# Kernel optimization log

Measured on AMD Instinct MI355X. Metric: run time of the kernel, lower is better.

Reference implementation:

```python
import jax, jax.numpy as jnp
import numpy as np

N_USER = 50000
N_ITEM = 100000
EMB = 64
NNZ = 1200000
BATCH = 4096
RATE = 0.1          # node_dropout[0]
N_LAYERS = 4        # len(layer_size); make_hop needs >=4 hops for 5 prefix means
N_NODES = N_USER + N_ITEM


def setup_inputs() -> dict:
    key = jax.random.key(0)
    ks = jax.random.split(key, 12)
    return {
        "user_emb": jax.random.normal(ks[0], (N_USER, EMB), dtype=jnp.float32) * 0.1,
        "item_emb": jax.random.normal(ks[1], (N_ITEM, EMB), dtype=jnp.float32) * 0.1,
        "adj_vals": jax.random.uniform(ks[2], (NNZ,), dtype=jnp.float32),
        "drop_u": jax.random.uniform(ks[3], (NNZ,), dtype=jnp.float32),
        "adj_rows": jax.random.randint(ks[4], (NNZ,), 0, N_NODES, dtype=jnp.int32),
        "adj_cols": jax.random.randint(ks[5], (NNZ,), 0, N_NODES, dtype=jnp.int32),
        "users": jax.random.randint(ks[6], (BATCH,), 0, N_USER, dtype=jnp.int32),
        "pos_items": jax.random.randint(ks[7], (BATCH,), 0, N_ITEM, dtype=jnp.int32),
        "neg_items": jax.random.randint(ks[8], (BATCH,), 0, N_ITEM, dtype=jnp.int32),
        "u_a": jax.random.randint(ks[9], (BATCH,), 0, 5, dtype=jnp.int32),
        "p_a": jax.random.randint(ks[10], (BATCH,), 0, 5, dtype=jnp.int32),
        "n_a": jax.random.randint(ks[11], (BATCH,), 0, 5, dtype=jnp.int32),
        "index": 0,
    }


def _make_hop(user_emb, item_emb, adj_vals, drop_u, adj_rows, adj_cols):
    # sparse dropout: floor(1 - rate + u) gives a 0/1 keep mask; rescale by 1/(1-rate).
    mask = jnp.floor((1.0 - RATE) + drop_u)
    vals = adj_vals * mask * (1.0 / (1.0 - RATE))
    ego = jnp.concatenate([user_emb, item_emb], axis=0)  # [N, d]
    all_embs = [ego]
    for _ in range(N_LAYERS):
        # SpMM: out[r] = sum_e vals[e] * ego[cols[e]] for rows[e] == r
        msgs = vals[:, None] * ego[adj_cols]             # [nnz, d]
        ego = jax.ops.segment_sum(msgs, adj_rows, num_segments=N_NODES)
        all_embs.append(ego)
    # prefix means over hops 0..i
    result = [all_embs[0]]
    running = all_embs[0]
    for i in range(1, 5):
        running = running + all_embs[i]
        result.append(running / float(i + 1))
    return jnp.stack(result)  # [5, N, d]


def reference(user_emb, item_emb, adj_vals, drop_u, adj_rows, adj_cols,
              users, pos_items, neg_items, u_a, p_a, n_a, index):
    embed = _make_hop(user_emb, item_emb, adj_vals, drop_u, adj_rows, adj_cols)
    n_user = user_emb.shape[0]
    if index == 0:
        u = embed[u_a, users]
        p = embed[p_a, pos_items + n_user]
        n = embed[n_a, neg_items + n_user]
    else:
        u = embed[u_a, users + n_user]
        p = embed[p_a, pos_items]
        n = embed[n_a, neg_items]
    return (u, p, n)
```

## Files before the change

kernel.cpp:

```cpp
#include <hip/hip_runtime.h>
#include <stdint.h>

#define N_USER_C  50000
#define N_ITEM_C  100000
#define N_NODES_C 150000
#define EMB_C     64
#define NNZ_C     1200000
#define BATCH_C   4096

#define BKT_SHIFT 9
#define BKT_ROWS  (1 << BKT_SHIFT)
#define NB        ((N_NODES_C + BKT_ROWS - 1) / BKT_ROWS)
#define CH        8192
#define NBLK      ((NNZ_C + CH - 1) / CH)
#define N2        (NB * NBLK)
#define COL_MASK  0x3FFFF

typedef _Float16 h16;
typedef _Float16 h16x4 __attribute__((ext_vector_type(4)));
typedef _Float16 h16x8 __attribute__((ext_vector_type(8)));

__global__ __launch_bounds__(1024) void k_bin_count(const float* __restrict__ du,
                                                    const int* __restrict__ rows,
                                                    int* __restrict__ cnt2) {
    __shared__ int bk[NB];
    int t = threadIdx.x, blk = blockIdx.x;
    for (int i = t; i < NB; i += 1024) bk[i] = 0;
    __syncthreads();
    int base = blk * CH;
    for (int i = 0; i < CH; i += 1024) {
        int e = base + i + t;
        if (e < NNZ_C && floorf(0.9f + du[e]) != 0.0f)
            atomicAdd(&bk[rows[e] >> BKT_SHIFT], 1);
    }
    __syncthreads();
    for (int i = t; i < NB; i += 1024) cnt2[i * NBLK + blk] = bk[i];
}

__global__ __launch_bounds__(256) void k_btot(const int* __restrict__ cnt2,
                                              int* __restrict__ btot) {
    __shared__ int red[256];
    int t = threadIdx.x, i = blockIdx.x;
    red[t] = (t < NBLK) ? cnt2[i * NBLK + t] : 0;
    __syncthreads();
    for (int off = 128; off > 0; off >>= 1) {
        if (t < off) red[t] += red[t + off];
        __syncthreads();
    }
    if (t == 0) btot[i] = red[0];
}

__global__ __launch_bounds__(512) void k_bbase(const int* __restrict__ btot,
                                               int* __restrict__ bbase,
                                               int* __restrict__ base2,
                                               int* __restrict__ row_start) {
    __shared__ int sh[512];
    int t = threadIdx.x;
    int v0 = (t < NB) ? btot[t] : 0;
    sh[t] = v0;
    __syncthreads();
    for (int off = 1; off < 512; off <<= 1) {
        int v = (t >= off) ? sh[t - off] : 0;
        __syncthreads();
        sh[t] += v;
        __syncthreads();
    }
    if (t < NB) bbase[t] = sh[t] - v0;
    if (t == 511) {
        base2[N2] = sh[511];
        row_start[N_NODES_C] = sh[511];
    }
}

__global__ __launch_bounds__(256) void k_bscan(const int* __restrict__ cnt2,
                                               const int* __restrict__ bbase,
                                               int* __restrict__ base2) {
    __shared__ int sh[256];
    int t = threadIdx.x, i = blockIdx.x;
    int v0 = (t < NBLK) ? cnt2[i * NBLK + t] : 0;
    sh[t] = v0;
    __syncthreads();
    for (int off = 1; off < 256; off <<= 1) {
        int v = (t >= off) ? sh[t - off] : 0;
        __syncthreads();
        sh[t] += v;
        __syncthreads();
    }
    if (t < NBLK) base2[i * NBLK + t] = bbase[i] + sh[t] - v0;
}

__global__ __launch_bounds__(1024) void k_bin_write(const float* __restrict__ av,
                                                    const float* __restrict__ du,
                                                    const int* __restrict__ rows,
                                                    const int* __restrict__ cols,
                                                    const int* __restrict__ base2,
                                                    int2* __restrict__ ev) {
    __shared__ int cur[NB];
    int t = threadIdx.x, blk = blockIdx.x;
    for (int i = t; i < NB; i += 1024) cur[i] = base2[i * NBLK + blk];
    __syncthreads();
    int base = blk * CH;
    for (int i = 0; i < CH; i += 1024) {
        int e = base + i + t;
        if (e < NNZ_C) {
            float m = floorf(0.9f + du[e]);
            if (m != 0.0f) {
                float v = av[e] * m * (float)(1.0 / 0.9);
                int r = rows[e];
                int pos = atomicAdd(&cur[r >> BKT_SHIFT], 1);
                int2 p;
                p.x = ((r & (BKT_ROWS - 1)) << 18) | cols[e];
                p.y = __float_as_int(v);
                ev[pos] = p;
            }
        }
    }
}

__global__ __launch_bounds__(256) void k_bucket_sort(const int2* __restrict__ ev,
                                                     const int* __restrict__ base2,
                                                     int2* __restrict__ ep,
                                                     int* __restrict__ row_start) {
    __shared__ int rowcnt[BKT_ROWS];
    __shared__ int cursor[BKT_ROWS];
    __shared__ int tsum[256];
    int t = threadIdx.x, k = blockIdx.x;
    int rowBase = k << BKT_SHIFT;
    int bstart = base2[k * NBLK];
    int bend   = base2[(k + 1) * NBLK];
    for (int i = t; i < BKT_ROWS; i += 256) rowcnt[i] = 0;
    __syncthreads();
    for (int e = bstart + t; e < bend; e += 256)
        atomicAdd(&rowcnt[((unsigned)ev[e].x) >> 18], 1);
    __syncthreads();
    int a = rowcnt[2 * t], b = rowcnt[2 * t + 1];
    tsum[t] = a + b;
    __syncthreads();
    for (int off = 1; off < 256; off <<= 1) {
        int v = (t >= off) ? tsum[t - off] : 0;
        __syncthreads();
        tsum[t] += v;
        __syncthreads();
    }
    int excl = tsum[t] - (a + b);
    cursor[2 * t]     = excl;
    cursor[2 * t + 1] = excl + a;
    int gr = rowBase + 2 * t;
    if (gr < N_NODES_C)     row_start[gr]     = bstart + excl;
    if (gr + 1 < N_NODES_C) row_start[gr + 1] = bstart + excl + a;
    __syncthreads();
    for (int e = bstart + t; e < bend; e += 256) {
        int2 p = ev[e];
        int rl = ((unsigned)p.x) >> 18;
        int slot = atomicAdd(&cursor[rl], 1);
        p.x &= COL_MASK;
        ep[bstart + slot] = p;
    }
}

__global__ __launch_bounds__(256) void k_tohalf(const float4* __restrict__ ue,
                                                const float4* __restrict__ ie,
                                                h16x4* __restrict__ dst) {
    const int totalU = N_USER_C * EMB_C / 4;
    const int total  = N_NODES_C * EMB_C / 4;
    int stride = gridDim.x * blockDim.x;
    for (int i = blockIdx.x * blockDim.x + threadIdx.x; i < total; i += stride) {
        float4 v = (i < totalU) ? ue[i] : ie[i - totalU];
        h16x4 h;
        h[0] = (h16)v.x; h[1] = (h16)v.y; h[2] = (h16)v.z; h[3] = (h16)v.w;
        dst[i] = h;
    }
}

__global__ __launch_bounds__(256) void k_spmm8d(const int* __restrict__ rs,
                                                const int2* __restrict__ ep,
                                                const h16x8* __restrict__ ego,
                                                h16x8* __restrict__ nxt,
                                                const int* __restrict__ flag) {
    int wid  = (blockIdx.x * blockDim.x + threadIdx.x) >> 6;
    int lane = threadIdx.x & 63;
    if (wid >= N_NODES_C) return;
    if (flag && flag[wid] == 0) return;
    int start = rs[wid];
    int end   = rs[wid + 1];
    int slot = lane >> 3;
    int q    = lane & 7;
    float acc[8] = {0.f, 0.f, 0.f, 0.f, 0.f, 0.f, 0.f, 0.f};
    #pragma unroll 2
    for (int it = start + slot; it < end; it += 8) {
        long long raw = __builtin_nontemporal_load((const long long*)(ep + it));
        int   c = (int)(raw & 0xFFFFFFFFLL);
        float v = __int_as_float((int)(raw >> 32));
        h16x8 g = ego[((int64_t)(c << 3)) + q];
        #pragma unroll
        for (int i = 0; i < 8; ++i) acc[i] += v * (float)g[i];
    }
    #pragma unroll
    for (int m = 8; m <= 32; m <<= 1) {
        #pragma unroll
        for (int i = 0; i < 8; ++i) acc[i] += __shfl_xor(acc[i], m);
    }
    if (lane < 8) {
        h16x8 h;
        #pragma unroll
        for (int i = 0; i < 8; ++i) h[i] = (h16)acc[i];
        nxt[(int64_t)wid * 8 + q] = h;
    }
}

__global__ __launch_bounds__(256) void k_flags(const int* __restrict__ rs,
                                               const int2* __restrict__ ep,
                                               int* __restrict__ flag,
                                               const int* __restrict__ users,
                                               const int* __restrict__ pos,
                                               const int* __restrict__ neg,
                                               const int* __restrict__ ua,
                                               const int* __restrict__ pa,
                                               const int* __restrict__ na,
                                               const int* __restrict__ indexp) {
    int wid  = (blockIdx.x * blockDim.x + threadIdx.x) >> 6;
    int lane = threadIdx.x & 63;
    if (wid >= 3 * BATCH_C) return;
    int s = wid >> 12;
    int j = wid & (BATCH_C - 1);
    int a = (s == 0) ? ua[j] : (s == 1) ? pa[j] : na[j];
    if (a < 3) return;
    int idx0 = indexp[0];
    int row;
    if (s == 0)      row = users[j] + (idx0 ? N_USER_C : 0);
    else if (s == 1) row = pos[j]   + (idx0 ? 0 : N_USER_C);
    else             row = neg[j]   + (idx0 ? 0 : N_USER_C);
    if (lane == 0) flag[row] = 1;
    if (a == 4) {
        int start = rs[row], end = rs[row + 1];
        for (int e = start + lane; e < end; e += 64)
            flag[ep[e].x] = 1;
    }
}

__global__ __launch_bounds__(256) void k_spmm_g4(const int* __restrict__ rs,
                                                 const int2* __restrict__ ep,
                                                 const h16x4* __restrict__ ego,
                                                 float* __restrict__ out,
                                                 const int* __restrict__ users,
                                                 const int* __restrict__ pos,
                                                 const int* __restrict__ neg,
                                                 const int* __restrict__ ua,
                                                 const int* __restrict__ pa,
                                                 const int* __restrict__ na,
                                                 const int* __restrict__ indexp) {
    int wid  = (blockIdx.x * blockDim.x + threadIdx.x) >> 6;
    int lane = threadIdx.x & 63;
    if (wid >= 3 * BATCH_C) return;
    int s = wid >> 12;
    int j = wid & (BATCH_C - 1);
    int a = (s == 0) ? ua[j] : (s == 1) ? pa[j] : na[j];
    if (a != 4) return;
    int idx0 = indexp[0];
    int row;
    if (s == 0)      row = users[j] + (idx0 ? N_USER_C : 0);
    else if (s == 1) row = pos[j]   + (idx0 ? 0 : N_USER_C);
    else             row = neg[j]   + (idx0 ? 0 : N_USER_C);
    int start = rs[row];
    int end   = rs[row + 1];
    int eo = lane >> 4;
    int l  = lane & 15;
    float4 acc = make_float4(0.f, 0.f, 0.f, 0.f);
    for (int it = start + eo; it < end; it += 4) {
        int2 p = ep[it];
        float v = __int_as_float(p.y);
        h16x4 g = ego[(int64_t)p.x * 16 + l];
        acc.x += v * (float)g[0]; acc.y += v * (float)g[1];
        acc.z += v * (float)g[2]; acc.w += v * (float)g[3];
    }
    acc.x += __shfl_xor(acc.x, 16); acc.y += __shfl_xor(acc.y, 16);
    acc.z += __shfl_xor(acc.z, 16); acc.w += __shfl_xor(acc.w, 16);
    acc.x += __shfl_xor(acc.x, 32); acc.y += __shfl_xor(acc.y, 32);
    acc.z += __shfl_xor(acc.z, 32); acc.w += __shfl_xor(acc.w, 32);
    if (lane < 16) {
        float4* o = (float4*)out + (int64_t)wid * 16 + l;
        float4 cv = *o;
        cv.x += acc.x; cv.y += acc.y; cv.z += acc.z; cv.w += acc.w;
        *o = cv;
    }
}

__global__ __launch_bounds__(256) void k_gather(const float* __restrict__ srcU,
                                                const float* __restrict__ srcI,
                                                int pivot,
                                                float* __restrict__ out,
                                                const int* __restrict__ users,
                                                const int* __restrict__ pos,
                                                const int* __restrict__ neg,
                                                const int* __restrict__ ua,
                                                const int* __restrict__ pa,
                                                const int* __restrict__ na,
                                                const int* __restrict__ indexp) {
    int t = blockIdx.x * blockDim.x + threadIdx.x;
    if (t >= 3 * BATCH_C * EMB_C) return;
    int d = t & 63;
    int b = t >> 6;
    int s = b >> 12;
    int j = b & (BATCH_C - 1);
    int idx0 = indexp[0];
    int row;
    if (s == 0)      row = users[j] + (idx0 ? N_USER_C : 0);
    else if (s == 1) row = pos[j]   + (idx0 ? 0 : N_USER_C);
    else             row = neg[j]   + (idx0 ? 0 : N_USER_C);
    const float* sp = (row < pivot) ? (srcU + (int64_t)row * EMB_C)
                                    : (srcI + (int64_t)(row - pivot) * EMB_C);
    out[t] = sp[d];
}

__global__ __launch_bounds__(256) void k_gather_h(const h16* __restrict__ src,
                                                  float* __restrict__ out,
                                                  const int* __restrict__ users,
                                                  const int* __restrict__ pos,
                                                  const int* __restrict__ neg,
                                                  const int* __restrict__ ua,
                                                  const int* __restrict__ pa,
                                                  const int* __restrict__ na,
                                                  const int* __restrict__ indexp,
                                                  int hop) {
    int t = blockIdx.x * blockDim.x + threadIdx.x;
    if (t >= 3 * BATCH_C * EMB_C) return;
    int d = t & 63;
    int b = t >> 6;
    int s = b >> 12;
    int j = b & (BATCH_C - 1);
    int idx0 = indexp[0];
    int row, a;
    if (s == 0)      { row = users[j] + (idx0 ? N_USER_C : 0); a = ua[j]; }
    else if (s == 1) { row = pos[j]   + (idx0 ? 0 : N_USER_C); a = pa[j]; }
    else             { row = neg[j]   + (idx0 ? 0 : N_USER_C); a = na[j]; }
    if (hop <= a)
        out[t] += (float)src[(int64_t)row * EMB_C + d];
}

__global__ __launch_bounds__(256) void k_scale(float* __restrict__ out,
                                               const int* __restrict__ ua,
                                               const int* __restrict__ pa,
                                               const int* __restrict__ na) {
    int t = blockIdx.x * blockDim.x + threadIdx.x;
    if (t >= 3 * BATCH_C * EMB_C) return;
    int b = t >> 6;
    int s = b >> 12;
    int j = b & (BATCH_C - 1);
    int a = (s == 0) ? ua[j] : (s == 1) ? pa[j] : na[j];
    out[t] /= (float)(a + 1);
}

extern "C" void kernel_launch(void* const* d_in, const int* in_sizes, int n_in,
                              void* d_out, int out_size, void* d_ws, size_t ws_size,
                              hipStream_t stream) {
    const float* user_emb = (const float*)d_in[0];
    const float* item_emb = (const float*)d_in[1];
    const float* adj_vals = (const float*)d_in[2];
    const float* drop_u   = (const float*)d_in[3];
    const int*   adj_rows = (const int*)d_in[4];
    const int*   adj_cols = (const int*)d_in[5];
    const int*   users    = (const int*)d_in[6];
    const int*   pos_it   = (const int*)d_in[7];
    const int*   neg_it   = (const int*)d_in[8];
    const int*   u_a      = (const int*)d_in[9];
    const int*   p_a      = (const int*)d_in[10];
    const int*   n_a      = (const int*)d_in[11];
    const int*   indexp   = (const int*)d_in[12];
    float* out = (float*)d_out;

    const size_t egoElems = (size_t)N_NODES_C * EMB_C;
    h16*   egoH0     = (h16*)d_ws;
    h16*   bufA      = egoH0 + egoElems;
    h16*   bufB      = bufA + egoElems;
    int2*  ep        = (int2*)(bufB + egoElems);
    int2*  ev        = ep + NNZ_C;
    int*   row_start = (int*)(ev + NNZ_C);
    int*   cnt2      = row_start + N_NODES_C + 1;
    int*   base2     = cnt2 + N2 + 1;
    int*   btot      = base2 + N2 + 1;
    int*   bbase     = btot + NB + 1;
    int*   flags     = bbase + NB + 1;

    k_bin_count<<<NBLK, 1024, 0, stream>>>(drop_u, adj_rows, cnt2);
    k_btot<<<NB, 256, 0, stream>>>(cnt2, btot);
    k_bbase<<<1, 512, 0, stream>>>(btot, bbase, base2, row_start);
    k_bscan<<<NB, 256, 0, stream>>>(cnt2, bbase, base2);
    k_bin_write<<<NBLK, 1024, 0, stream>>>(adj_vals, drop_u, adj_rows, adj_cols,
                                           base2, ev);
    k_bucket_sort<<<NB, 256, 0, stream>>>(ev, base2, ep, row_start);

    hipMemsetAsync(flags, 0, N_NODES_C * sizeof(int), stream);
    k_flags<<<(3 * BATCH_C * 64 + 255) / 256, 256, 0, stream>>>(
        row_start, ep, flags, users, pos_it, neg_it, u_a, p_a, n_a, indexp);

    k_tohalf<<<2048, 256, 0, stream>>>((const float4*)user_emb,
                                       (const float4*)item_emb, (h16x4*)egoH0);
    const int GT = 3 * BATCH_C * EMB_C;
    k_gather<<<(GT + 255) / 256, 256, 0, stream>>>(user_emb, item_emb, N_USER_C, out,
                                                   users, pos_it, neg_it,
                                                   u_a, p_a, n_a, indexp);

    const int SPMM_BLOCKS = (N_NODES_C * 64 + 255) / 256;
    k_spmm8d<<<SPMM_BLOCKS, 256, 0, stream>>>(row_start, ep, (const h16x8*)egoH0,
                                              (h16x8*)bufA, (const int*)nullptr);
    k_gather_h<<<(GT + 255) / 256, 256, 0, stream>>>(bufA, out, users, pos_it, neg_it,
                                                     u_a, p_a, n_a, indexp, 1);
    k_spmm8d<<<SPMM_BLOCKS, 256, 0, stream>>>(row_start, ep, (const h16x8*)bufA,
                                              (h16x8*)bufB, (const int*)nullptr);
    k_gather_h<<<(GT + 255) / 256, 256, 0, stream>>>(bufB, out, users, pos_it, neg_it,
                                                     u_a, p_a, n_a, indexp, 2);
    k_spmm8d<<<SPMM_BLOCKS, 256, 0, stream>>>(row_start, ep, (const h16x8*)bufB,
                                              (h16x8*)bufA, flags);
    k_gather_h<<<(GT + 255) / 256, 256, 0, stream>>>(bufA, out, users, pos_it, neg_it,
                                                     u_a, p_a, n_a, indexp, 3);
    k_spmm_g4<<<(3 * BATCH_C * 64 + 255) / 256, 256, 0, stream>>>(
        row_start, ep, (const h16x4*)bufA, out,
        users, pos_it, neg_it, u_a, p_a, n_a, indexp);

    k_scale<<<(GT + 255) / 256, 256, 0, stream>>>(out, u_a, p_a, n_a);
}
```

Measured before the change: 214.4 us.

## Prune layer-2 SpMM to rows needed downstream and switch to 16-lane mapping

Adds a second flag set marking rows needed at hop 2 (batch rows with hop>=2 and neighbours of hop-3 rows), computed by a new propagation kernel, and restricts the second SpMM to those rows. Also changes the SpMM lane mapping from 8 edges x 8 lanes with 16-byte loads to 4 edges x 16 lanes with 8-byte loads and drops the nontemporal edge load. Costs an extra flag-propagation launch and a larger memset; the remapping may reduce per-lane load width.

```diff
diff --git a/kernel.cpp b/kernel.cpp
--- a/kernel.cpp
+++ b/kernel.cpp
@@ -18,7 +18,6 @@
 
 typedef _Float16 h16;
 typedef _Float16 h16x4 __attribute__((ext_vector_type(4)));
-typedef _Float16 h16x8 __attribute__((ext_vector_type(8)));
 
 __global__ __launch_bounds__(1024) void k_bin_count(const float* __restrict__ du,
                                                     const int* __restrict__ rows,
@@ -172,10 +171,10 @@
     }
 }
 
-__global__ __launch_bounds__(256) void k_spmm8d(const int* __restrict__ rs,
+__global__ __launch_bounds__(256) void k_spmm_h(const int* __restrict__ rs,
                                                 const int2* __restrict__ ep,
-                                                const h16x8* __restrict__ ego,
-                                                h16x8* __restrict__ nxt,
+                                                const h16x4* __restrict__ ego,
+                                                h16x4* __restrict__ nxt,
                                                 const int* __restrict__ flag) {
     int wid  = (blockIdx.x * blockDim.x + threadIdx.x) >> 6;
     int lane = threadIdx.x & 63;
@@ -183,34 +182,32 @@
     if (flag && flag[wid] == 0) return;
     int start = rs[wid];
     int end   = rs[wid + 1];
-    int slot = lane >> 3;
-    int q    = lane & 7;
-    float acc[8] = {0.f, 0.f, 0.f, 0.f, 0.f, 0.f, 0.f, 0.f};
+    int eo = lane >> 4;
+    int l  = lane & 15;
+    float4 acc = make_float4(0.f, 0.f, 0.f, 0.f);
     #pragma unroll 2
-    for (int it = start + slot; it < end; it += 8) {
-        long long raw = __builtin_nontemporal_load((const long long*)(ep + it));
-        int   c = (int)(raw & 0xFFFFFFFFLL);
-        float v = __int_as_float((int)(raw >> 32));
-        h16x8 g = ego[((int64_t)(c << 3)) + q];
-        #pragma unroll
-        for (int i = 0; i < 8; ++i) acc[i] += v * (float)g[i];
-    }
-    #pragma unroll
-    for (int m = 8; m <= 32; m <<= 1) {
-        #pragma unroll
-        for (int i = 0; i < 8; ++i) acc[i] += __shfl_xor(acc[i], m);
-    }
-    if (lane < 8) {
-        h16x8 h;
-        #pragma unroll
-        for (int i = 0; i < 8; ++i) h[i] = (h16)acc[i];
-        nxt[(int64_t)wid * 8 + q] = h;
+    for (int it = start + eo; it < end; it += 4) {
+        int2 p = ep[it];
+        float v = __int_as_float(p.y);
+        h16x4 g = ego[(int64_t)p.x * 16 + l];
+        acc.x += v * (float)g[0]; acc.y += v * (float)g[1];
+        acc.z += v * (float)g[2]; acc.w += v * (float)g[3];
+    }
+    acc.x += __shfl_xor(acc.x, 16); acc.y += __shfl_xor(acc.y, 16);
+    acc.z += __shfl_xor(acc.z, 16); acc.w += __shfl_xor(acc.w, 16);
+    acc.x += __shfl_xor(acc.x, 32); acc.y += __shfl_xor(acc.y, 32);
+    acc.z += __shfl_xor(acc.z, 32); acc.w += __shfl_xor(acc.w, 32);
+    if (lane < 16) {
+        h16x4 h;
+        h[0] = (h16)acc.x; h[1] = (h16)acc.y; h[2] = (h16)acc.z; h[3] = (h16)acc.w;
+        nxt[(int64_t)wid * 16 + l] = h;
     }
 }
 
 __global__ __launch_bounds__(256) void k_flags(const int* __restrict__ rs,
                                                const int2* __restrict__ ep,
-                                               int* __restrict__ flag,
+                                               int* __restrict__ flag3,
+                                               int* __restrict__ flag2,
                                                const int* __restrict__ users,
                                                const int* __restrict__ pos,
                                                const int* __restrict__ neg,
@@ -224,18 +221,34 @@
     int s = wid >> 12;
     int j = wid & (BATCH_C - 1);
     int a = (s == 0) ? ua[j] : (s == 1) ? pa[j] : na[j];
-    if (a < 3) return;
+    if (a < 2) return;
     int idx0 = indexp[0];
     int row;
     if (s == 0)      row = users[j] + (idx0 ? N_USER_C : 0);
     else if (s == 1) row = pos[j]   + (idx0 ? 0 : N_USER_C);
     else             row = neg[j]   + (idx0 ? 0 : N_USER_C);
-    if (lane == 0) flag[row] = 1;
+    if (lane == 0) {
+        flag2[row] = 1;
+        if (a >= 3) flag3[row] = 1;
+    }
     if (a == 4) {
         int start = rs[row], end = rs[row + 1];
         for (int e = start + lane; e < end; e += 64)
-            flag[ep[e].x] = 1;
-    }
+            flag3[ep[e].x] = 1;
+    }
+}
+
+__global__ __launch_bounds__(256) void k_flags2(const int* __restrict__ rs,
+                                                const int2* __restrict__ ep,
+                                                const int* __restrict__ flag3,
+                                                int* __restrict__ flag2) {
+    int wid  = (blockIdx.x * blockDim.x + threadIdx.x) >> 6;
+    int lane = threadIdx.x & 63;
+    if (wid >= N_NODES_C) return;
+    if (flag3[wid] == 0) return;
+    int start = rs[wid], end = rs[wid + 1];
+    for (int e = start + lane; e < end; e += 64)
+        flag2[ep[e].x] = 1;
 }
 
 __global__ __launch_bounds__(256) void k_spmm_g4(const int* __restrict__ rs,
@@ -379,7 +392,8 @@
     int*   base2     = cnt2 + N2 + 1;
     int*   btot      = base2 + N2 + 1;
     int*   bbase     = btot + NB + 1;
-    int*   flags     = bbase + NB + 1;
+    int*   flags3    = bbase + NB + 1;
+    int*   flags2    = flags3 + N_NODES_C;
 
     k_bin_count<<<NBLK, 1024, 0, stream>>>(drop_u, adj_rows, cnt2);
     k_btot<<<NB, 256, 0, stream>>>(cnt2, btot);
@@ -389,9 +403,11 @@
                                            base2, ev);
     k_bucket_sort<<<NB, 256, 0, stream>>>(ev, base2, ep, row_start);
 
-    hipMemsetAsync(flags, 0, N_NODES_C * sizeof(int), stream);
+    hipMemsetAsync(flags3, 0, 2 * N_NODES_C * sizeof(int), stream);
     k_flags<<<(3 * BATCH_C * 64 + 255) / 256, 256, 0, stream>>>(
-        row_start, ep, flags, users, pos_it, neg_it, u_a, p_a, n_a, indexp);
+        row_start, ep, flags3, flags2, users, pos_it, neg_it, u_a, p_a, n_a, indexp);
+    k_flags2<<<(N_NODES_C * 64 + 255) / 256, 256, 0, stream>>>(
+        row_start, ep, flags3, flags2);
 
     k_tohalf<<<2048, 256, 0, stream>>>((const float4*)user_emb,
                                        (const float4*)item_emb, (h16x4*)egoH0);
@@ -401,16 +417,16 @@
                                                    u_a, p_a, n_a, indexp);
 
     const int SPMM_BLOCKS = (N_NODES_C * 64 + 255) / 256;
-    k_spmm8d<<<SPMM_BLOCKS, 256, 0, stream>>>(row_start, ep, (const h16x8*)egoH0,
-                                              (h16x8*)bufA, (const int*)nullptr);
+    k_spmm_h<<<SPMM_BLOCKS, 256, 0, stream>>>(row_start, ep, (const h16x4*)egoH0,
+                                              (h16x4*)bufA, (const int*)nullptr);
     k_gather_h<<<(GT + 255) / 256, 256, 0, stream>>>(bufA, out, users, pos_it, neg_it,
                                                      u_a, p_a, n_a, indexp, 1);
-    k_spmm8d<<<SPMM_BLOCKS, 256, 0, stream>>>(row_start, ep, (const h16x8*)bufA,
-                                              (h16x8*)bufB, (const int*)nullptr);
+    k_spmm_h<<<SPMM_BLOCKS, 256, 0, stream>>>(row_start, ep, (const h16x4*)bufA,
+                                              (h16x4*)bufB, flags2);
     k_gather_h<<<(GT + 255) / 256, 256, 0, stream>>>(bufB, out, users, pos_it, neg_it,
                                                      u_a, p_a, n_a, indexp, 2);
-    k_spmm8d<<<SPMM_BLOCKS, 256, 0, stream>>>(row_start, ep, (const h16x8*)bufB,
-                                              (h16x8*)bufA, flags);
+    k_spmm_h<<<SPMM_BLOCKS, 256, 0, stream>>>(row_start, ep, (const h16x4*)bufB,
+                                              (h16x4*)bufA, flags3);
     k_gather_h<<<(GT + 255) / 256, 256, 0, stream>>>(bufA, out, users, pos_it, neg_it,
                                                      u_a, p_a, n_a, indexp, 3);
     k_spmm_g4<<<(3 * BATCH_C * 64 + 255) / 256, 256, 0, stream>>>(
```

New measurement: 211.2 us. Within noise of the previous version (-1.5%).
